# Performance work log

Hardware: AMD Instinct MI355X
Metric: run time of the kernel (lower is better)

## Reference

```python
import jax, jax.numpy as jnp
import numpy as np

B, N, K = 32, 64, 128          # batch, atoms per cell, channel width (128x0e + 128x1o)
R_MAX = 5.0
NUM_BESSEL = 8
P_CUT = 5                       # num_polynomial_cutoff
AVG_NEIGH = 16.0                # avg_num_neighbors
H_MLP = 512                     # hidden_dimensions_size, n_hidden_dimensions = 2
FEAT = 5 * K                    # ((num_interactions-1)*4 + 1) * 128 = 640


def silu(x):
    return x * jax.nn.sigmoid(x)


def _bessel_cutoff(r, mask):
    # Bessel radial basis * polynomial cutoff (MACE), masked on valid edges.
    n = jnp.arange(1, NUM_BESSEL + 1, dtype=r.dtype)
    rb = jnp.sqrt(2.0 / R_MAX) * jnp.sin(n * (jnp.pi / R_MAX) * r[..., None]) / r[..., None]
    u = r / R_MAX
    p = float(P_CUT)
    fc = 1.0 - 0.5 * (p + 1) * (p + 2) * u**P_CUT + p * (p + 2) * u**(P_CUT + 1) - 0.5 * p * (p + 1) * u**(P_CUT + 2)
    fc = fc * (u < 1.0)
    return rb * (fc * mask)[..., None]


def _sph(uvec):
    # Real spherical harmonics l=0,1,2 (component normalization), uvec: unit edge vectors.
    x, y, z = uvec[..., 0], uvec[..., 1], uvec[..., 2]
    s3, s5, s15 = 3.0**0.5, 5.0**0.5, 15.0**0.5
    Y0 = jnp.ones_like(x)[..., None]
    Y1 = jnp.stack([s3 * x, s3 * y, s3 * z], -1)
    Y2 = jnp.stack([s15 * x * y, s15 * y * z, 0.5 * s5 * (3 * z * z - 1.0),
                    s15 * x * z, 0.5 * s15 * (x * x - y * y)], -1)
    return Y0, Y1, Y2


def _radial_mlp(x, w0, b0, w1, b1, w2, b2, w3, b3):
    h = silu(x @ w0 + b0)
    h = silu(h @ w1 + b1)
    h = silu(h @ w2 + b2)
    return h @ w3 + b3


def setup_inputs() -> dict:
    key = jax.random.key(0)
    ks = jax.random.split(key, 32)
    f32 = jnp.float32

    def lin(k, fan_in, shape):
        return (jax.random.normal(k, shape, dtype=f32) / np.sqrt(fan_in)).astype(f32)

    inp = {
        "noisy_relative_positions": jax.random.uniform(ks[0], (B, N, 3), dtype=f32),
        "time": jax.random.uniform(ks[1], (B, 1), dtype=f32),
        "unit_cell": (11.0 * jnp.eye(3, dtype=f32) + 0.3 * jax.random.uniform(ks[2], (B, 3, 3), dtype=f32)),
        "w_embed": lin(ks[3], 1, (K,)),
        # interaction 1 radial MLP: 8 -> 64 -> 64 -> 64 -> 3*K (weights for l=0,1,2 paths)
        "r1_w0": lin(ks[4], NUM_BESSEL, (NUM_BESSEL, 64)), "r1_b0": jnp.zeros((64,), f32),
        "r1_w1": lin(ks[5], 64, (64, 64)), "r1_b1": jnp.zeros((64,), f32),
        "r1_w2": lin(ks[6], 64, (64, 64)), "r1_b2": jnp.zeros((64,), f32),
        "r1_w3": lin(ks[7], 64, (64, 3 * K)), "r1_b3": jnp.zeros((3 * K,), f32),
        "mix1_l0": lin(ks[8], K, (K, K)),
        "mix1_l1": lin(ks[9], K, (K, K)),
        "mix1_l2": lin(ks[10], K, (K, K)),
        # interaction 2 radial MLP: 8 -> 64 -> 64 -> 64 -> 2*K (paths 0e x 0e -> 0e, 1o x 1o -> 0e)
        "r2_w0": lin(ks[11], NUM_BESSEL, (NUM_BESSEL, 64)), "r2_b0": jnp.zeros((64,), f32),
        "r2_w1": lin(ks[12], 64, (64, 64)), "r2_b1": jnp.zeros((64,), f32),
        "r2_w2": lin(ks[13], 64, (64, 64)), "r2_b2": jnp.zeros((64,), f32),
        "r2_w3": lin(ks[14], 64, (64, 2 * K)), "r2_b3": jnp.zeros((2 * K,), f32),
        "mix2": lin(ks[15], K, (K, K)),
        # readout MLP: 641 -> 512 -> 512 -> 3
        "mlp_w0": lin(ks[16], FEAT + 1, (FEAT + 1, H_MLP)), "mlp_b0": jnp.zeros((H_MLP,), f32),
        "mlp_w1": lin(ks[17], H_MLP, (H_MLP, H_MLP)), "mlp_b1": jnp.zeros((H_MLP,), f32),
        "mlp_w2": lin(ks[18], H_MLP, (H_MLP, 3)), "mlp_b2": jnp.zeros((3,), f32),
    }
    return inp


def reference(noisy_relative_positions, time, unit_cell, w_embed,
              r1_w0, r1_b0, r1_w1, r1_b1, r1_w2, r1_b2, r1_w3, r1_b3,
              mix1_l0, mix1_l1, mix1_l2,
              r2_w0, r2_b0, r2_w1, r2_b1, r2_w2, r2_b2, r2_w3, r2_b3, mix2,
              mlp_w0, mlp_b0, mlp_w1, mlp_b1, mlp_w2, mlp_b2):
    frac = noisy_relative_positions                      # [B,N,3] fractional
    d = frac[:, :, None, :] - frac[:, None, :, :]        # [B,N,N,3]
    d = d - jnp.round(d)                                 # minimum-image PBC
    dc = jnp.einsum('bijc,bcd->bijd', d, unit_cell)      # cartesian displacements
    r = jnp.sqrt(jnp.maximum(jnp.sum(dc * dc, -1), 1e-12))
    mask = (r < R_MAX) & (~jnp.eye(N, dtype=bool))[None]
    r_safe = jnp.where(mask, r, 1.0)
    uvec = dc / r_safe[..., None] * mask[..., None]      # unit edge vectors (0 off-edge)

    rad = _bessel_cutoff(r_safe, mask)                   # [B,N,N,8]
    Y0, Y1, Y2 = _sph(uvec)                              # [B,N,N,1|3|5]

    h0 = jnp.broadcast_to(w_embed, (B, N, K))            # element embedding (single species)

    # ---- interaction 1: radial-weighted tensor product h_j (x) Y_l, scatter over j ----
    we = _radial_mlp(rad, r1_w0, r1_b0, r1_w1, r1_b1, r1_w2, r1_b2, r1_w3, r1_b3)
    we = we.reshape(B, N, N, 3, K) * mask[..., None, None]
    hj = h0[:, None, :, :]                               # sender features [B,1,N,K]
    msg0 = jnp.einsum('bijk,bijm->bimk', we[..., 0, :] * hj, Y0)[:, :, 0] / AVG_NEIGH  # [B,N,K]
    msg1 = jnp.einsum('bijk,bijm->bimk', we[..., 1, :] * hj, Y1) / AVG_NEIGH           # [B,N,3,K]
    msg2 = jnp.einsum('bijk,bijm->bimk', we[..., 2, :] * hj, Y2) / AVG_NEIGH           # [B,N,5,K]

    s1 = msg0 @ mix1_l0 + jnp.sum(msg2 * msg2, axis=2) @ mix1_l2   # scalars [B,N,K]
    v1 = jnp.einsum('bimk,kc->bimc', msg1, mix1_l1)                # vectors [B,N,3,K]
    h1 = silu(s1)

    # ---- interaction 2: scalar output from 0e x 0e and 1o x 1o -> 0e paths ----
    we2 = _radial_mlp(rad, r2_w0, r2_b0, r2_w1, r2_b1, r2_w2, r2_b2, r2_w3, r2_b3)
    we2 = we2.reshape(B, N, N, 2, K) * mask[..., None, None]
    msg_a = jnp.sum(we2[..., 0, :] * h1[:, None, :, :], axis=2)    # [B,N,K]
    inv = jnp.einsum('bijm,bjmk->bijk', Y1, v1)                    # Y1 . v1_j invariant
    msg_b = jnp.sum(we2[..., 1, :] * inv, axis=2)
    s2 = ((msg_a + msg_b) / AVG_NEIGH) @ mix2                      # [B,N,K]

    # node_feats: layer1 full irreps (128x0e + 128x1o -> 512) + layer2 scalars (128) = 640
    node_feats = jnp.concatenate([s1, v1.reshape(B, N, 3 * K), s2], axis=-1)

    t = jnp.broadcast_to(time[:, None, :], (B, N, 1))
    x = jnp.concatenate([node_feats, t], axis=-1)                  # [B,N,641]
    x = jax.nn.relu(x @ mlp_w0 + mlp_b0)
    x = jax.nn.relu(x @ mlp_w1 + mlp_b1)
    return x @ mlp_w2 + mlp_b2                                     # [B,N,3]
```

## Files before the change

kernel.cpp:

```cpp
#include <hip/hip_runtime.h>
#include <math.h>

#define B_ 32
#define N_ 64
#define K_ 128
#define NPAIR (B_*N_*N_)
#define PREP_TOTAL 733184

typedef __attribute__((ext_vector_type(8))) short short8;
typedef __attribute__((ext_vector_type(8))) __bf16 bf16x8;
typedef __attribute__((ext_vector_type(4))) float floatx4;

__device__ __forceinline__ float silu_f(float x) {
    return x / (1.0f + __expf(-x));
}

__device__ __forceinline__ short f2bf(float x) {
    union { float f; unsigned u; } v; v.f = x;
    unsigned r = (v.u + 0x7FFFu + ((v.u >> 16) & 1u)) >> 16;
    return (short)r;
}
__device__ __forceinline__ float bf2f(short s) {
    union { unsigned u; float f; } v;
    v.u = ((unsigned)(unsigned short)s) << 16;
    return v.f;
}
__device__ __forceinline__ bf16x8 ld_frag(const short* p) {
    short8 r = *(const short8*)p;
    return __builtin_bit_cast(bf16x8, r);
}

__global__ __launch_bounds__(256) void prep_kernel(
    const float* __restrict__ r1w1, const float* __restrict__ r1w2,
    const float* __restrict__ r2w1, const float* __restrict__ r2w2,
    const float* __restrict__ r2w3, const float* __restrict__ mw0,
    const float* __restrict__ mw1,
    const float* __restrict__ r1w0, const float* __restrict__ r2w0,
    const float* __restrict__ r1w3,
    const float* __restrict__ l0, const float* __restrict__ l1,
    const float* __restrict__ l2,
    short* __restrict__ dst)
{
    int idx = blockIdx.x * 256 + threadIdx.x;
    if (idx >= PREP_TOTAL) return;
    short v;
    if (idx < 4096) {
        int h = idx >> 6, k = idx & 63; v = f2bf(r1w1[k*64 + h]);
    } else if (idx < 8192) {
        int i = idx - 4096; int h = i >> 6, k = i & 63; v = f2bf(r1w2[k*64 + h]);
    } else if (idx < 12288) {
        int i = idx - 8192; int h = i >> 6, k = i & 63; v = f2bf(r2w1[k*64 + h]);
    } else if (idx < 16384) {
        int i = idx - 12288; int h = i >> 6, k = i & 63; v = f2bf(r2w2[k*64 + h]);
    } else if (idx < 32768) {
        int i = idx - 16384; int col = i >> 6, h = i & 63; v = f2bf(r2w3[h*256 + col]);
    } else if (idx < 393216) {
        int i = idx - 32768; int n = i / 704, k = i - n*704;
        v = (k < 641) ? f2bf(mw0[(size_t)k*512 + n]) : (short)0;
    } else if (idx < 655360) {
        int i = idx - 393216; int n = i >> 9, k = i & 511;
        v = f2bf(mw1[(size_t)k*512 + n]);
    } else if (idx < 657408) {
        int i = idx - 655360; int h = i >> 5, k = i & 31;
        v = (k < 8) ? f2bf(r1w0[k*64 + h]) : (short)0;
    } else if (idx < 659456) {
        int i = idx - 657408; int h = i >> 5, k = i & 31;
        v = (k < 8) ? f2bf(r2w0[k*64 + h]) : (short)0;
    } else if (idx < 684032) {
        int i = idx - 659456; int col = i >> 6, h = i & 63;
        v = f2bf(r1w3[(size_t)h*384 + col]);
    } else {
        int i = idx - 684032; int n = i >> 7, k = i & 127;
        float src = (n < 128) ? l0[(size_t)k*128 + n]
                  : (n < 256) ? l1[(size_t)k*128 + (n-128)]
                              : l2[(size_t)k*128 + (n-256)];
        v = f2bf(src);
    }
    dst[idx] = v;
}

__device__ __forceinline__ void mfma_layer(
    const short* __restrict__ src, const short* __restrict__ WT,
    const float* __restrict__ bias, short* __restrict__ dst,
    int wv, int qd, int nn)
{
    floatx4 acc[4];
    #pragma unroll
    for (int tt = 0; tt < 4; tt++) acc[tt] = (floatx4){0.f, 0.f, 0.f, 0.f};
    #pragma unroll
    for (int ks = 0; ks < 64; ks += 32) {
        bf16x8 a = ld_frag(&src[(wv*16 + nn)*72 + ks + qd*8]);
        #pragma unroll
        for (int tt = 0; tt < 4; tt++) {
            bf16x8 b = ld_frag(&WT[(tt*16 + nn)*64 + ks + qd*8]);
            acc[tt] = __builtin_amdgcn_mfma_f32_16x16x32_bf16(a, b, acc[tt], 0, 0, 0);
        }
    }
    #pragma unroll
    for (int tt = 0; tt < 4; tt++) {
        int col = tt*16 + nn;
        float bv = bias[col];
        #pragma unroll
        for (int i = 0; i < 4; i++) {
            int row = wv*16 + qd*4 + i;
            dst[row*72 + col] = f2bf(silu_f(acc[tt][i] + bv));
        }
    }
}

__device__ __forceinline__ void mfma_layer_T(
    const short* __restrict__ src, const short* __restrict__ WT,
    const float* __restrict__ bias, short* __restrict__ dstT,
    int wv, int qd, int nn)
{
    floatx4 acc[4];
    #pragma unroll
    for (int tt = 0; tt < 4; tt++) acc[tt] = (floatx4){0.f, 0.f, 0.f, 0.f};
    #pragma unroll
    for (int ks = 0; ks < 64; ks += 32) {
        bf16x8 a = ld_frag(&src[(wv*16 + nn)*72 + ks + qd*8]);
        #pragma unroll
        for (int tt = 0; tt < 4; tt++) {
            bf16x8 b = ld_frag(&WT[(tt*16 + nn)*64 + ks + qd*8]);
            acc[tt] = __builtin_amdgcn_mfma_f32_16x16x32_bf16(a, b, acc[tt], 0, 0, 0);
        }
    }
    #pragma unroll
    for (int tt = 0; tt < 4; tt++) {
        int col = tt*16 + nn;
        float bv = bias[col];
        #pragma unroll
        for (int i = 0; i < 4; i++) {
            int row = wv*16 + qd*4 + i;
            dstT[col*72 + row] = f2bf(silu_f(acc[tt][i] + bv));
        }
    }
}

__device__ __forceinline__ void mfma_layer_gout(
    const short* __restrict__ src, const short* __restrict__ WT,
    const float* __restrict__ bias, short* __restrict__ gdst,
    int wv, int qd, int nn)
{
    floatx4 acc[4];
    #pragma unroll
    for (int tt = 0; tt < 4; tt++) acc[tt] = (floatx4){0.f, 0.f, 0.f, 0.f};
    #pragma unroll
    for (int ks = 0; ks < 64; ks += 32) {
        bf16x8 a = ld_frag(&src[(wv*16 + nn)*72 + ks + qd*8]);
        #pragma unroll
        for (int tt = 0; tt < 4; tt++) {
            bf16x8 b = ld_frag(&WT[(tt*16 + nn)*64 + ks + qd*8]);
            acc[tt] = __builtin_amdgcn_mfma_f32_16x16x32_bf16(a, b, acc[tt], 0, 0, 0);
        }
    }
    #pragma unroll
    for (int tt = 0; tt < 4; tt++) {
        int col = tt*16 + nn;
        float bv = bias[col];
        #pragma unroll
        for (int i = 0; i < 4; i++) {
            int row = wv*16 + qd*4 + i;
            gdst[row*64 + col] = f2bf(silu_f(acc[tt][i] + bv));
        }
    }
}

__device__ __forceinline__ void mfma_layer0(
    const short* __restrict__ rad_bf, const short* __restrict__ w0T,
    const float* __restrict__ b0, short* __restrict__ dst,
    int wv, int qd, int nn)
{
    floatx4 acc[4];
    #pragma unroll
    for (int tt = 0; tt < 4; tt++) acc[tt] = (floatx4){0.f, 0.f, 0.f, 0.f};
    bf16x8 a = ld_frag(&rad_bf[(wv*16 + nn)*32 + qd*8]);
    #pragma unroll
    for (int tt = 0; tt < 4; tt++) {
        bf16x8 b = ld_frag(&w0T[(tt*16 + nn)*32 + qd*8]);
        acc[tt] = __builtin_amdgcn_mfma_f32_16x16x32_bf16(a, b, acc[tt], 0, 0, 0);
    }
    #pragma unroll
    for (int tt = 0; tt < 4; tt++) {
        int col = tt*16 + nn;
        float bv = b0[col];
        #pragma unroll
        for (int i = 0; i < 4; i++) {
            int row = wv*16 + qd*4 + i;
            dst[row*72 + col] = f2bf(silu_f(acc[tt][i] + bv));
        }
    }
}

__global__ __launch_bounds__(256) void mlpx_kernel(
    const float* __restrict__ pos, const float* __restrict__ cell,
    const short* __restrict__ w0T1, const float* __restrict__ b01,
    const short* __restrict__ w1T1, const float* __restrict__ b11,
    const short* __restrict__ w2T1, const float* __restrict__ b21,
    const short* __restrict__ w0T2, const float* __restrict__ b02,
    const short* __restrict__ w1T2, const float* __restrict__ b12,
    const short* __restrict__ w2T2, const float* __restrict__ b22,
    float* __restrict__ geo4, short* __restrict__ hc2, short* __restrict__ Gg)
{
    __shared__ __align__(16) short actA[64*72];
    __shared__ __align__(16) short actB[64*72];
    __shared__ __align__(16) short rad_bf[64*32];
    __shared__ __align__(16) short Ym_bf[16*72];
    int t = threadIdx.x;
    int wv = t >> 6, lane = t & 63, qd = lane >> 4, nn = lane & 15;
    int node = blockIdx.x;
    int b = node >> 6;
    int irow = node & 63;
    size_t pbase = (size_t)node * 64;

    if (t < 64) {
        int j = t;
        const float* pi = pos + (size_t)(b*N_ + irow)*3;
        const float* pj = pos + (size_t)(b*N_ + j)*3;
        float d0 = pi[0]-pj[0], d1 = pi[1]-pj[1], d2 = pi[2]-pj[2];
        d0 -= rintf(d0); d1 -= rintf(d1); d2 -= rintf(d2);
        const float* C = cell + b*9;
        float dc0 = d0*C[0] + d1*C[3] + d2*C[6];
        float dc1 = d0*C[1] + d1*C[4] + d2*C[7];
        float dc2 = d0*C[2] + d1*C[5] + d2*C[8];
        float r2 = fmaxf(dc0*dc0 + dc1*dc1 + dc2*dc2, 1e-12f);
        float r = sqrtf(r2);
        bool m = (r < 5.0f) && (irow != j);
        float mf = m ? 1.0f : 0.0f;
        float rs = m ? r : 1.0f;
        float inv_rs = 1.0f / rs;
        float x = dc0*inv_rs*mf, y = dc1*inv_rs*mf, z = dc2*inv_rs*mf;
        float u = r * 0.2f;
        float u2 = u*u, u4 = u2*u2, u5 = u4*u;
        float fc = 1.0f - 21.0f*u5 + 35.0f*u5*u - 15.0f*u5*u2;
        fc = (u < 1.0f) ? fc : 0.0f;
        float pref = 0.6324555320336759f * inv_rs * (fc * mf);
        float w = 0.6283185307179586f * rs;
        float sw = sinf(w), cw = cosf(w);
        float twoc = 2.0f * cw;
        float sm = 0.0f, s = sw;
        #pragma unroll
        for (int n = 0; n < 8; n++) {
            rad_bf[j*32 + n] = f2bf(pref * s);
            float nx = twoc*s - sm;
            sm = s; s = nx;
        }
        #pragma unroll
        for (int k = 8; k < 32; k++) rad_bf[j*32 + k] = 0;
        const float s3  = 1.7320508075688772f;
        const float s5  = 2.23606797749979f;
        const float s15 = 3.872983346207417f;
        float vals[9];
        vals[0] = mf;
        vals[1] = s3*x; vals[2] = s3*y; vals[3] = s3*z;
        vals[4] = s15*x*y;
        vals[5] = s15*y*z;
        vals[6] = 0.5f*s5*(3.0f*z*z - 1.0f);
        vals[7] = s15*x*z;
        vals[8] = 0.5f*s15*(x*x - y*y);
        *(float4*)&geo4[(pbase + j)*4] = make_float4(mf, vals[1], vals[2], vals[3]);
        #pragma unroll
        for (int m9 = 0; m9 < 9; m9++) Ym_bf[m9*72 + j] = f2bf(vals[m9]);
        #pragma unroll
        for (int m9 = 9; m9 < 16; m9++) Ym_bf[m9*72 + j] = 0;
        #pragma unroll
        for (int m9 = 0; m9 < 9; m9++) {
            float sv = vals[m9];
            #pragma unroll
            for (int off = 32; off > 0; off >>= 1) sv += __shfl_xor(sv, off);
            if (j == m9)
                *(float*)(Gg + (size_t)node*1152 + m9*72 + 64) = sv;
        }
    }
    __syncthreads();

    mfma_layer0(rad_bf, w0T2, b02, actA, wv, qd, nn);
    __syncthreads();

    mfma_layer(actA, w1T2, b12, actB, wv, qd, nn);
    __syncthreads();

    mfma_layer_gout(actB, w2T2, b22, hc2 + (size_t)node*4096, wv, qd, nn);
    mfma_layer0(rad_bf, w0T1, b01, actA, wv, qd, nn);
    __syncthreads();

    mfma_layer(actA, w1T1, b11, actB, wv, qd, nn);
    __syncthreads();

    mfma_layer_T(actB, w2T1, b21, actA, wv, qd, nn);
    __syncthreads();

    {
        floatx4 acc = (floatx4){0.f, 0.f, 0.f, 0.f};
        #pragma unroll
        for (int ks = 0; ks < 64; ks += 32) {
            bf16x8 a = ld_frag(&Ym_bf[nn*72 + ks + qd*8]);
            bf16x8 bb = ld_frag(&actA[(wv*16 + nn)*72 + ks + qd*8]);
            acc = __builtin_amdgcn_mfma_f32_16x16x32_bf16(a, bb, acc, 0, 0, 0);
        }
        #pragma unroll
        for (int i = 0; i < 4; i++)
            Gg[(size_t)node*1152 + (qd*4 + i)*72 + wv*16 + nn] = f2bf(acc[i]);
    }
}

__global__ __launch_bounds__(256) void back1_kernel(
    const float* __restrict__ wemb,
    const short* __restrict__ Gg,
    const short* __restrict__ w3T, const float* __restrict__ b3,
    const short* __restrict__ lcatT, const float* __restrict__ timeg,
    float* __restrict__ h1g, float* __restrict__ v1g, short* __restrict__ featsb)
{
    __shared__ __align__(16) short G_lds[16*72];
    __shared__ __align__(16) short A2[16*136];
    __shared__ float q_s[128];
    __shared__ float Ps[256];
    int t = threadIdx.x;
    int wv = t >> 6, lane = t & 63, qd = lane >> 4, nn = lane & 15;
    int node = blockIdx.x;
    int b = node >> 6;

    if (t < 144)
        ((uint4*)G_lds)[t] = ((const uint4*)(Gg + (size_t)node*1152))[t];
    if (t < 128) q_s[t] = 0.f;
    for (int z = 680 + t; z < 2176; z += 256) A2[z] = 0;
    __syncthreads();

    {
        bf16x8 ga0 = ld_frag(&G_lds[nn*72 + qd*8]);
        bf16x8 ga1 = ld_frag(&G_lds[nn*72 + 32 + qd*8]);
        floatx4 acc[6];
        #pragma unroll
        for (int tt = 0; tt < 6; tt++) acc[tt] = (floatx4){0.f, 0.f, 0.f, 0.f};
        #pragma unroll
        for (int tt = 0; tt < 6; tt++) {
            int tn = wv*6 + tt;
            bf16x8 b0f = ld_frag(&w3T[(tn*16 + nn)*64 + qd*8]);
            bf16x8 b1f = ld_frag(&w3T[(tn*16 + nn)*64 + 32 + qd*8]);
            acc[tt] = __builtin_amdgcn_mfma_f32_16x16x32_bf16(ga0, b0f, acc[tt], 0, 0, 0);
            acc[tt] = __builtin_amdgcn_mfma_f32_16x16x32_bf16(ga1, b1f, acc[tt], 0, 0, 0);
        }
        #pragma unroll
        for (int tt = 0; tt < 6; tt++) {
            int col = (wv*6 + tt)*16 + nn;
            #pragma unroll
            for (int i = 0; i < 4; i++) {
                int m9 = qd*4 + i;
                if (m9 < 9) {
                    int c = (m9 == 0) ? 0 : ((m9 < 4) ? 1 : 2);
                    int k = col - c*128;
                    if (k >= 0 && k < 128) {
                        float sym = *(const float*)(&G_lds[m9*72 + 64]);
                        float val = (acc[tt][i] + sym*b3[col]) * wemb[k] * 0.0625f;
                        if (m9 == 0)      A2[k] = f2bf(val);
                        else if (m9 < 4)  A2[(m9+1)*136 + k] = f2bf(val);
                        else              atomicAdd(&q_s[k], val*val);
                    }
                }
            }
        }
    }
    __syncthreads();

    if (t < 128) A2[136 + t] = f2bf(q_s[t]);
    __syncthreads();

    {
        bf16x8 pa[4];
        #pragma unroll
        for (int ksI = 0; ksI < 4; ksI++)
            pa[ksI] = ld_frag(&A2[nn*136 + ksI*32 + qd*8]);
        floatx4 acc[6];
        #pragma unroll
        for (int tt = 0; tt < 6; tt++) acc[tt] = (floatx4){0.f, 0.f, 0.f, 0.f};
        #pragma unroll
        for (int tt = 0; tt < 6; tt++) {
            int tn = wv*6 + tt;
            #pragma unroll
            for (int ksI = 0; ksI < 4; ksI++) {
                bf16x8 bf = ld_frag(&lcatT[((size_t)(tn*16 + nn))*128 + ksI*32 + qd*8]);
                acc[tt] = __builtin_amdgcn_mfma_f32_16x16x32_bf16(pa[ksI], bf, acc[tt], 0, 0, 0);
            }
        }
        #pragma unroll
        for (int tt = 0; tt < 6; tt++) {
            int n = (wv*6 + tt)*16 + nn;
            #pragma unroll
            for (int i = 0; i < 4; i++) {
                int r = qd*4 + i;
                float val = acc[tt][i];
                if (r == 0 && n < 128) Ps[n] = val;
                else if (r == 1 && n >= 256) Ps[128 + n - 256] = val;
                else if (r >= 2 && r < 5 && n >= 128 && n < 256) {
                    int m9 = r - 2, cc = n - 128;
                    v1g[(size_t)node*384 + m9*128 + cc] = val;
                    featsb[(size_t)node*704 + 128 + m9*128 + cc] = f2bf(val);
                }
            }
        }
    }
    __syncthreads();

    if (t < 128) {
        float s1 = Ps[t] + Ps[128 + t];
        featsb[(size_t)node*704 + t] = f2bf(s1);
        h1g[(size_t)node*128 + t] = silu_f(s1);
    } else if (t == 128) {
        featsb[(size_t)node*704 + 640] = f2bf(timeg[b]);
    } else if (t > 128 && t < 192) {
        featsb[(size_t)node*704 + 640 + (t - 128)] = 0;
    }
}

__global__ __launch_bounds__(256) void pass2b_kernel(
    const float* __restrict__ geo4,
    const short* __restrict__ hc2,
    const short* __restrict__ w3T, const float* __restrict__ b3,
    const float* __restrict__ mix2,
    const float* __restrict__ h1g, const float* __restrict__ v1g,
    short* __restrict__ featsb)
{
    __shared__ float mask_s[64];
    __shared__ float Y1s[64*4];
    __shared__ float msgab[128];
    int t = threadIdx.x;
    int wv = t >> 6, lane = t & 63, qd = lane >> 4, nn = lane & 15;
    int node = blockIdx.x;
    int b = node >> 6;
    size_t pbase = (size_t)node * 64;

    if (t < 64) {
        float4 g = *(const float4*)&geo4[(pbase + t)*4];
        mask_s[t] = g.x;
        Y1s[t*4 + 0] = g.y; Y1s[t*4 + 1] = g.z; Y1s[t*4 + 2] = g.w;
    }
    if (t >= 64 && t < 192) msgab[t - 64] = 0.f;
    __syncthreads();

    const short* hcb = hc2 + (size_t)node*4096;
    bf16x8 a0 = ld_frag(&hcb[(wv*16 + nn)*64 + qd*8]);
    bf16x8 a1 = ld_frag(&hcb[(wv*16 + nn)*64 + 32 + qd*8]);
    for (int g = 0; g < 4; g++) {
        floatx4 acc[4];
        #pragma unroll
        for (int tt = 0; tt < 4; tt++) acc[tt] = (floatx4){0.f, 0.f, 0.f, 0.f};
        #pragma unroll
        for (int tt = 0; tt < 4; tt++) {
            int ct = g*4 + tt;
            bf16x8 b0f = ld_frag(&w3T[(ct*16 + nn)*64 + qd*8]);
            bf16x8 b1f = ld_frag(&w3T[(ct*16 + nn)*64 + 32 + qd*8]);
            acc[tt] = __builtin_amdgcn_mfma_f32_16x16x32_bf16(a0, b0f, acc[tt], 0, 0, 0);
            acc[tt] = __builtin_amdgcn_mfma_f32_16x16x32_bf16(a1, b1f, acc[tt], 0, 0, 0);
        }
        #pragma unroll
        for (int tt = 0; tt < 4; tt++) {
            int col = (g*4 + tt)*16 + nn;
            float bias = b3[col];
            int k = col & 127;
            float p = 0.f;
            if (col < 128) {
                #pragma unroll
                for (int i = 0; i < 4; i++) {
                    int j = wv*16 + qd*4 + i;
                    float we = (acc[tt][i] + bias) * mask_s[j];
                    p += we * h1g[((size_t)b*64 + j)*128 + k];
                }
            } else {
                #pragma unroll
                for (int i = 0; i < 4; i++) {
                    int j = wv*16 + qd*4 + i;
                    float we = (acc[tt][i] + bias) * mask_s[j];
                    const float* vb = &v1g[((size_t)b*64 + j)*384 + k];
                    float inv = Y1s[j*4+0]*vb[0] + Y1s[j*4+1]*vb[128] + Y1s[j*4+2]*vb[256];
                    p += we * inv;
                }
            }
            p += __shfl_xor(p, 16);
            p += __shfl_xor(p, 32);
            if (qd == 0) atomicAdd(&msgab[k], p);
        }
    }
    __syncthreads();

    if (t < 128) {
        int c = t;
        float acc = 0.f;
        for (int k = 0; k < 128; k++) acc += msgab[k] * mix2[k*128 + c];
        featsb[(size_t)node*704 + 512 + c] = f2bf(acc * 0.0625f);
    }
}

__global__ __launch_bounds__(256) void gemm_mfma_kernel(
    const short* __restrict__ A, int lda,
    const short* __restrict__ BT, int ldb, int K,
    const float* __restrict__ bias, short* __restrict__ Cout, int ldo)
{
    __shared__ short As[64*72];
    __shared__ short Bs[64*72];
    int t = threadIdx.x;
    int wv = t >> 6, lane = t & 63, qd = lane >> 4, nn = lane & 15;
    int m0 = blockIdx.x * 64, n0 = blockIdx.y * 64;
    floatx4 acc[4];
    #pragma unroll
    for (int tt = 0; tt < 4; tt++) acc[tt] = (floatx4){0.f, 0.f, 0.f, 0.f};

    for (int kc = 0; kc < K; kc += 64) {
        for (int s = t; s < 512; s += 256) {
            int j = s >> 3, kk = (s & 7) * 8;
            *(uint4*)&As[j*72 + kk] = *(const uint4*)&A[(size_t)(m0 + j)*lda + kc + kk];
            *(uint4*)&Bs[j*72 + kk] = *(const uint4*)&BT[(size_t)(n0 + j)*ldb + kc + kk];
        }
        __syncthreads();
        #pragma unroll
        for (int ks = 0; ks < 64; ks += 32) {
            bf16x8 a = ld_frag(&As[(wv*16 + nn)*72 + ks + qd*8]);
            #pragma unroll
            for (int tt = 0; tt < 4; tt++) {
                bf16x8 bb = ld_frag(&Bs[(tt*16 + nn)*72 + ks + qd*8]);
                acc[tt] = __builtin_amdgcn_mfma_f32_16x16x32_bf16(a, bb, acc[tt], 0, 0, 0);
            }
        }
        __syncthreads();
    }
    #pragma unroll
    for (int tt = 0; tt < 4; tt++) {
        int n = n0 + tt*16 + nn;
        float bv = bias[n];
        #pragma unroll
        for (int i = 0; i < 4; i++) {
            int m = m0 + wv*16 + qd*4 + i;
            Cout[(size_t)m*ldo + n] = f2bf(fmaxf(acc[tt][i] + bv, 0.f));
        }
    }
}

__global__ __launch_bounds__(64) void final3_kernel(
    const short* __restrict__ H, const float* __restrict__ w2,
    const float* __restrict__ b2, float* __restrict__ out)
{
    int node = blockIdx.x, lane = threadIdx.x;
    float a0 = 0.f, a1 = 0.f, a2 = 0.f;
    #pragma unroll
    for (int r = 0; r < 8; r++) {
        int k = r*64 + lane;
        float h = bf2f(H[(size_t)node*512 + k]);
        a0 += h * w2[k*3 + 0];
        a1 += h * w2[k*3 + 1];
        a2 += h * w2[k*3 + 2];
    }
    #pragma unroll
    for (int off = 32; off > 0; off >>= 1) {
        a0 += __shfl_down(a0, off);
        a1 += __shfl_down(a1, off);
        a2 += __shfl_down(a2, off);
    }
    if (lane == 0) {
        out[(size_t)node*3 + 0] = a0 + b2[0];
        out[(size_t)node*3 + 1] = a1 + b2[1];
        out[(size_t)node*3 + 2] = a2 + b2[2];
    }
}

extern "C" void kernel_launch(void* const* d_in, const int* in_sizes, int n_in,
                              void* d_out, int out_size, void* d_ws, size_t ws_size,
                              hipStream_t stream) {
    const float* pos   = (const float*)d_in[0];
    const float* timeg = (const float*)d_in[1];
    const float* cell  = (const float*)d_in[2];
    const float* wemb  = (const float*)d_in[3];
    const float* r1w0  = (const float*)d_in[4];
    const float* r1b0  = (const float*)d_in[5];
    const float* r1w1  = (const float*)d_in[6];
    const float* r1b1  = (const float*)d_in[7];
    const float* r1w2  = (const float*)d_in[8];
    const float* r1b2  = (const float*)d_in[9];
    const float* r1w3  = (const float*)d_in[10];
    const float* r1b3  = (const float*)d_in[11];
    const float* l0    = (const float*)d_in[12];
    const float* l1    = (const float*)d_in[13];
    const float* l2    = (const float*)d_in[14];
    const float* r2w0  = (const float*)d_in[15];
    const float* r2b0  = (const float*)d_in[16];
    const float* r2w1  = (const float*)d_in[17];
    const float* r2b1  = (const float*)d_in[18];
    const float* r2w2  = (const float*)d_in[19];
    const float* r2b2  = (const float*)d_in[20];
    const float* r2w3  = (const float*)d_in[21];
    const float* r2b3  = (const float*)d_in[22];
    const float* mix2  = (const float*)d_in[23];
    const float* mw0   = (const float*)d_in[24];
    const float* mb0   = (const float*)d_in[25];
    const float* mw1   = (const float*)d_in[26];
    const float* mb1   = (const float*)d_in[27];
    const float* mw2   = (const float*)d_in[28];
    const float* mb2   = (const float*)d_in[29];

    float* ws    = (float*)d_ws;
    float* geo4  = ws;
    float* h1    = geo4 + (size_t)NPAIR*4;
    float* v1    = h1   + (size_t)B_*N_*K_;
    short* featsb = (short*)(v1 + (size_t)B_*N_*3*K_);
    short* prep  = featsb + (size_t)2048*704;
    short* w1T_1 = prep;
    short* w2T_1 = prep + 4096;
    short* w1T_2 = prep + 8192;
    short* w2T_2 = prep + 12288;
    short* w3T_2 = prep + 16384;
    short* wT0   = prep + 32768;
    short* wT1   = prep + 393216;
    short* w0T_1 = prep + 655360;
    short* w0T_2 = prep + 657408;
    short* w3T_1 = prep + 659456;
    short* lcatT = prep + 684032;
    short* hc2   = prep + PREP_TOTAL;
    short* Gg    = hc2 + (size_t)2048*4096;
    short* h0bb  = hc2;
    short* h1bb  = hc2 + (size_t)2048*512;

    prep_kernel<<<(PREP_TOTAL + 255)/256, 256, 0, stream>>>(
        r1w1, r1w2, r2w1, r2w2, r2w3, mw0, mw1,
        r1w0, r2w0, r1w3, l0, l1, l2, prep);
    mlpx_kernel<<<B_*N_, 256, 0, stream>>>(pos, cell,
        w0T_1, r1b0, w1T_1, r1b1, w2T_1, r1b2,
        w0T_2, r2b0, w1T_2, r2b1, w2T_2, r2b2,
        geo4, hc2, Gg);
    back1_kernel<<<B_*N_, 256, 0, stream>>>(wemb, Gg,
        w3T_1, r1b3, lcatT, timeg, h1, v1, featsb);
    pass2b_kernel<<<B_*N_, 256, 0, stream>>>(geo4, hc2,
        w3T_2, r2b3, mix2, h1, v1, featsb);
    dim3 g0(32, 8);
    gemm_mfma_kernel<<<g0, 256, 0, stream>>>(featsb, 704, wT0, 704, 704, mb0, h0bb, 512);
    gemm_mfma_kernel<<<g0, 256, 0, stream>>>(h0bb, 512, wT1, 512, 512, mb1, h1bb, 512);
    final3_kernel<<<B_*N_, 64, 0, stream>>>(h1bb, mw2, mb2, (float*)d_out);
}
```

Measured before the change: 289.1 us.

## Merge all stages into one persistent cooperative kernel with grid syncs

The seven separate launches (weight prep, radial MLPs, two interaction passes, two GEMMs, final projection) become one persistent cooperative kernel. Blocks loop over nodes or tiles in each stage and are separated by grid-wide barriers, with shared memory carved from one buffer. The aim is to remove per-launch overhead and the tail gaps between kernels. In exchange, the grid is capped at occupancy times 256 CUs, so each block handles several nodes serially and every stage is bound by the slowest block before the barrier. If the cooperative launch fails, the original multi-kernel path runs instead.

```diff
diff --git a/kernel.cpp b/kernel.cpp
--- a/kernel.cpp
+++ b/kernel.cpp
@@ -1,5 +1,8 @@
 #include <hip/hip_runtime.h>
+#include <hip/hip_cooperative_groups.h>
 #include <math.h>
+
+namespace cg = cooperative_groups;
 
 #define B_ 32
 #define N_ 64
@@ -30,7 +33,8 @@
     return __builtin_bit_cast(bf16x8, r);
 }
 
-__global__ __launch_bounds__(256) void prep_kernel(
+
+__device__ __forceinline__ void prep_elem(int idx,
     const float* __restrict__ r1w1, const float* __restrict__ r1w2,
     const float* __restrict__ r2w1, const float* __restrict__ r2w2,
     const float* __restrict__ r2w3, const float* __restrict__ mw0,
@@ -41,8 +45,6 @@
     const float* __restrict__ l2,
     short* __restrict__ dst)
 {
-    int idx = blockIdx.x * 256 + threadIdx.x;
-    if (idx >= PREP_TOTAL) return;
     short v;
     if (idx < 4096) {
         int h = idx >> 6, k = idx & 63; v = f2bf(r1w1[k*64 + h]);
@@ -192,7 +194,7 @@
     }
 }
 
-__global__ __launch_bounds__(256) void mlpx_kernel(
+__device__ __forceinline__ void mlpx_body(int node, char* sm,
     const float* __restrict__ pos, const float* __restrict__ cell,
     const short* __restrict__ w0T1, const float* __restrict__ b01,
     const short* __restrict__ w1T1, const float* __restrict__ b11,
@@ -202,16 +204,18 @@
     const short* __restrict__ w2T2, const float* __restrict__ b22,
     float* __restrict__ geo4, short* __restrict__ hc2, short* __restrict__ Gg)
 {
-    __shared__ __align__(16) short actA[64*72];
-    __shared__ __align__(16) short actB[64*72];
-    __shared__ __align__(16) short rad_bf[64*32];
-    __shared__ __align__(16) short Ym_bf[16*72];
+    short* actA   = (short*)sm;
+    short* actB   = (short*)(sm + 9216);
+    short* rad_bf = (short*)(sm + 18432);
+    short* Ym_bf  = (short*)(sm + 22528);
+
     int t = threadIdx.x;
     int wv = t >> 6, lane = t & 63, qd = lane >> 4, nn = lane & 15;
-    int node = blockIdx.x;
     int b = node >> 6;
     int irow = node & 63;
     size_t pbase = (size_t)node * 64;
+
+    __syncthreads();
 
     if (t < 64) {
         int j = t;
@@ -238,12 +242,12 @@
         float w = 0.6283185307179586f * rs;
         float sw = sinf(w), cw = cosf(w);
         float twoc = 2.0f * cw;
-        float sm = 0.0f, s = sw;
+        float sm2 = 0.0f, s = sw;
         #pragma unroll
         for (int n = 0; n < 8; n++) {
             rad_bf[j*32 + n] = f2bf(pref * s);
-            float nx = twoc*s - sm;
-            sm = s; s = nx;
+            float nx = twoc*s - sm2;
+            sm2 = s; s = nx;
         }
         #pragma unroll
         for (int k = 8; k < 32; k++) rad_bf[j*32 + k] = 0;
@@ -276,20 +280,15 @@
 
     mfma_layer0(rad_bf, w0T2, b02, actA, wv, qd, nn);
     __syncthreads();
-
     mfma_layer(actA, w1T2, b12, actB, wv, qd, nn);
     __syncthreads();
-
     mfma_layer_gout(actB, w2T2, b22, hc2 + (size_t)node*4096, wv, qd, nn);
     mfma_layer0(rad_bf, w0T1, b01, actA, wv, qd, nn);
     __syncthreads();
-
     mfma_layer(actA, w1T1, b11, actB, wv, qd, nn);
     __syncthreads();
-
     mfma_layer_T(actB, w2T1, b21, actA, wv, qd, nn);
     __syncthreads();
-
     {
         floatx4 acc = (floatx4){0.f, 0.f, 0.f, 0.f};
         #pragma unroll
@@ -304,21 +303,22 @@
     }
 }
 
-__global__ __launch_bounds__(256) void back1_kernel(
+__device__ __forceinline__ void back1_body(int node, char* sm,
     const float* __restrict__ wemb,
     const short* __restrict__ Gg,
     const short* __restrict__ w3T, const float* __restrict__ b3,
     const short* __restrict__ lcatT, const float* __restrict__ timeg,
     float* __restrict__ h1g, float* __restrict__ v1g, short* __restrict__ featsb)
 {
-    __shared__ __align__(16) short G_lds[16*72];
-    __shared__ __align__(16) short A2[16*136];
-    __shared__ float q_s[128];
-    __shared__ float Ps[256];
+    short* G_lds = (short*)sm;
+    short* A2    = (short*)(sm + 2304);
+    float* q_s   = (float*)(sm + 6656);
+    float* Ps    = (float*)(sm + 7168);
     int t = threadIdx.x;
     int wv = t >> 6, lane = t & 63, qd = lane >> 4, nn = lane & 15;
-    int node = blockIdx.x;
     int b = node >> 6;
+
+    __syncthreads();
 
     if (t < 144)
         ((uint4*)G_lds)[t] = ((const uint4*)(Gg + (size_t)node*1152))[t];
@@ -412,7 +412,7 @@
     }
 }
 
-__global__ __launch_bounds__(256) void pass2b_kernel(
+__device__ __forceinline__ void pass2b_body(int node, char* sm,
     const float* __restrict__ geo4,
     const short* __restrict__ hc2,
     const short* __restrict__ w3T, const float* __restrict__ b3,
@@ -420,14 +420,15 @@
     const float* __restrict__ h1g, const float* __restrict__ v1g,
     short* __restrict__ featsb)
 {
-    __shared__ float mask_s[64];
-    __shared__ float Y1s[64*4];
-    __shared__ float msgab[128];
+    float* mask_s = (float*)sm;
+    float* Y1s    = (float*)(sm + 256);
+    float* msgab  = (float*)(sm + 1280);
     int t = threadIdx.x;
     int wv = t >> 6, lane = t & 63, qd = lane >> 4, nn = lane & 15;
-    int node = blockIdx.x;
     int b = node >> 6;
     size_t pbase = (size_t)node * 64;
+
+    __syncthreads();
 
     if (t < 64) {
         float4 g = *(const float4*)&geo4[(pbase + t)*4];
@@ -490,21 +491,21 @@
     }
 }
 
-__global__ __launch_bounds__(256) void gemm_mfma_kernel(
+__device__ __forceinline__ void gemm_body(int m0, int n0, char* sm,
     const short* __restrict__ A, int lda,
     const short* __restrict__ BT, int ldb, int K,
     const float* __restrict__ bias, short* __restrict__ Cout, int ldo)
 {
-    __shared__ short As[64*72];
-    __shared__ short Bs[64*72];
+    short* As = (short*)sm;
+    short* Bs = (short*)(sm + 9216);
     int t = threadIdx.x;
     int wv = t >> 6, lane = t & 63, qd = lane >> 4, nn = lane & 15;
-    int m0 = blockIdx.x * 64, n0 = blockIdx.y * 64;
     floatx4 acc[4];
     #pragma unroll
     for (int tt = 0; tt < 4; tt++) acc[tt] = (floatx4){0.f, 0.f, 0.f, 0.f};
 
     for (int kc = 0; kc < K; kc += 64) {
+        __syncthreads();
         for (int s = t; s < 512; s += 256) {
             int j = s >> 3, kk = (s & 7) * 8;
             *(uint4*)&As[j*72 + kk] = *(const uint4*)&A[(size_t)(m0 + j)*lda + kc + kk];
@@ -520,8 +521,8 @@
                 acc[tt] = __builtin_amdgcn_mfma_f32_16x16x32_bf16(a, bb, acc[tt], 0, 0, 0);
             }
         }
-        __syncthreads();
-    }
+    }
+    __syncthreads();
     #pragma unroll
     for (int tt = 0; tt < 4; tt++) {
         int n = n0 + tt*16 + nn;
@@ -534,11 +535,10 @@
     }
 }
 
-__global__ __launch_bounds__(64) void final3_kernel(
+__device__ __forceinline__ void final3_body(int node, int lane,
     const short* __restrict__ H, const float* __restrict__ w2,
     const float* __restrict__ b2, float* __restrict__ out)
 {
-    int node = blockIdx.x, lane = threadIdx.x;
     float a0 = 0.f, a1 = 0.f, a2 = 0.f;
     #pragma unroll
     for (int r = 0; r < 8; r++) {
@@ -558,6 +558,146 @@
         out[(size_t)node*3 + 0] = a0 + b2[0];
         out[(size_t)node*3 + 1] = a1 + b2[1];
         out[(size_t)node*3 + 2] = a2 + b2[2];
+    }
+}
+
+__global__ __launch_bounds__(256) void prep_kernel(
+    const float* r1w1, const float* r1w2, const float* r2w1, const float* r2w2,
+    const float* r2w3, const float* mw0, const float* mw1,
+    const float* r1w0, const float* r2w0, const float* r1w3,
+    const float* l0, const float* l1, const float* l2, short* dst)
+{
+    int idx = blockIdx.x * 256 + threadIdx.x;
+    if (idx >= PREP_TOTAL) return;
+    prep_elem(idx, r1w1, r1w2, r2w1, r2w2, r2w3, mw0, mw1, r1w0, r2w0, r1w3,
+              l0, l1, l2, dst);
+}
+
+__global__ __launch_bounds__(256) void mlpx_kernel(
+    const float* pos, const float* cell,
+    const short* w0T1, const float* b01, const short* w1T1, const float* b11,
+    const short* w2T1, const float* b21,
+    const short* w0T2, const float* b02, const short* w1T2, const float* b12,
+    const short* w2T2, const float* b22,
+    float* geo4, short* hc2, short* Gg)
+{
+    __shared__ __align__(16) char sm[24832];
+    mlpx_body(blockIdx.x, sm, pos, cell, w0T1, b01, w1T1, b11, w2T1, b21,
+              w0T2, b02, w1T2, b12, w2T2, b22, geo4, hc2, Gg);
+}
+
+__global__ __launch_bounds__(256) void back1_kernel(
+    const float* wemb, const short* Gg, const short* w3T, const float* b3,
+    const short* lcatT, const float* timeg,
+    float* h1g, float* v1g, short* featsb)
+{
+    __shared__ __align__(16) char sm[8192];
+    back1_body(blockIdx.x, sm, wemb, Gg, w3T, b3, lcatT, timeg, h1g, v1g, featsb);
+}
+
+__global__ __launch_bounds__(256) void pass2b_kernel(
+    const float* geo4, const short* hc2, const short* w3T, const float* b3,
+    const float* mix2, const float* h1g, const float* v1g, short* featsb)
+{
+    __shared__ __align__(16) char sm[1792];
+    pass2b_body(blockIdx.x, sm, geo4, hc2, w3T, b3, mix2, h1g, v1g, featsb);
+}
+
+__global__ __launch_bounds__(256) void gemm_mfma_kernel(
+    const short* A, int lda, const short* BT, int ldb, int K,
+    const float* bias, short* Cout, int ldo)
+{
+    __shared__ __align__(16) char sm[18432];
+    gemm_body(blockIdx.x * 64, blockIdx.y * 64, sm, A, lda, BT, ldb, K, bias, Cout, ldo);
+}
+
+__global__ __launch_bounds__(64) void final3_kernel(
+    const short* H, const float* w2, const float* b2, float* out)
+{
+    final3_body(blockIdx.x, threadIdx.x, H, w2, b2, out);
+}
+
+__global__ __launch_bounds__(256) void mega_kernel(
+    const float* pos, const float* timeg, const float* cell, const float* wemb,
+    const float* r1w0, const float* r1b0, const float* r1w1, const float* r1b1,
+    const float* r1w2, const float* r1b2, const float* r1w3, const float* r1b3,
+    const float* l0, const float* l1, const float* l2,
+    const float* r2w0, const float* r2b0, const float* r2w1, const float* r2b1,
+    const float* r2w2, const float* r2b2, const float* r2w3, const float* r2b3,
+    const float* mix2,
+    const float* mw0, const float* mb0, const float* mw1, const float* mb1,
+    const float* mw2, const float* mb2,
+    float* ws, float* outp)
+{
+    cg::grid_group grid = cg::this_grid();
+    __shared__ __align__(16) char sm[24832];
+    const int G = (int)gridDim.x;
+    int t = threadIdx.x;
+
+    float* geo4  = ws;
+    float* h1    = geo4 + (size_t)NPAIR*4;
+    float* v1    = h1   + (size_t)B_*N_*K_;
+    short* featsb = (short*)(v1 + (size_t)B_*N_*3*K_);
+    short* prep  = featsb + (size_t)2048*704;
+    short* w1T_1 = prep;
+    short* w2T_1 = prep + 4096;
+    short* w1T_2 = prep + 8192;
+    short* w2T_2 = prep + 12288;
+    short* w3T_2 = prep + 16384;
+    short* wT0   = prep + 32768;
+    short* wT1   = prep + 393216;
+    short* w0T_1 = prep + 655360;
+    short* w0T_2 = prep + 657408;
+    short* w3T_1 = prep + 659456;
+    short* lcatT = prep + 684032;
+    short* hc2   = prep + PREP_TOTAL;
+    short* Gg    = hc2 + (size_t)2048*4096;
+    short* h0bb  = hc2;
+    short* h1bb  = hc2 + (size_t)2048*512;
+
+    for (int idx = blockIdx.x*256 + t; idx < PREP_TOTAL; idx += G*256)
+        prep_elem(idx, r1w1, r1w2, r2w1, r2w2, r2w3, mw0, mw1, r1w0, r2w0, r1w3,
+                  l0, l1, l2, prep);
+    __threadfence();
+    grid.sync();
+
+    for (int node = blockIdx.x; node < 2048; node += G)
+        mlpx_body(node, sm, pos, cell, w0T_1, r1b0, w1T_1, r1b1, w2T_1, r1b2,
+                  w0T_2, r2b0, w1T_2, r2b1, w2T_2, r2b2, geo4, hc2, Gg);
+    __threadfence();
+    grid.sync();
+
+    for (int node = blockIdx.x; node < 2048; node += G)
+        back1_body(node, sm, wemb, Gg, w3T_1, r1b3, lcatT, timeg, h1, v1, featsb);
+    __threadfence();
+    grid.sync();
+
+    for (int node = blockIdx.x; node < 2048; node += G)
+        pass2b_body(node, sm, geo4, hc2, w3T_2, r2b3, mix2, h1, v1, featsb);
+    __threadfence();
+    grid.sync();
+
+    for (int tile = blockIdx.x; tile < 256; tile += G) {
+        int m0 = (tile & 31) * 64, n0 = (tile >> 5) * 64;
+        gemm_body(m0, n0, sm, featsb, 704, wT0, 704, 704, mb0, h0bb, 512);
+    }
+    __threadfence();
+    grid.sync();
+
+    for (int tile = blockIdx.x; tile < 256; tile += G) {
+        int m0 = (tile & 31) * 64, n0 = (tile >> 5) * 64;
+        gemm_body(m0, n0, sm, h0bb, 512, wT1, 512, 512, mb1, h1bb, 512);
+    }
+    __threadfence();
+    grid.sync();
+
+    {
+        int wv = t >> 6, lane = t & 63;
+        for (int base = blockIdx.x*4; base < 2048; base += G*4) {
+            int node = base + wv;
+            if (node < 2048)
+                final3_body(node, lane, h1bb, mw2, mb2, outp);
+        }
     }
 }
 
@@ -596,6 +736,7 @@
     const float* mb2   = (const float*)d_in[29];
 
     float* ws    = (float*)d_ws;
+    float* outp  = (float*)d_out;
     float* geo4  = ws;
     float* h1    = geo4 + (size_t)NPAIR*4;
     float* v1    = h1   + (size_t)B_*N_*K_;
@@ -617,19 +758,48 @@
     short* h0bb  = hc2;
     short* h1bb  = hc2 + (size_t)2048*512;
 
-    prep_kernel<<<(PREP_TOTAL + 255)/256, 256, 0, stream>>>(
-        r1w1, r1w2, r2w1, r2w2, r2w3, mw0, mw1,
-        r1w0, r2w0, r1w3, l0, l1, l2, prep);
-    mlpx_kernel<<<B_*N_, 256, 0, stream>>>(pos, cell,
-        w0T_1, r1b0, w1T_1, r1b1, w2T_1, r1b2,
-        w0T_2, r2b0, w1T_2, r2b1, w2T_2, r2b2,
-        geo4, hc2, Gg);
-    back1_kernel<<<B_*N_, 256, 0, stream>>>(wemb, Gg,
-        w3T_1, r1b3, lcatT, timeg, h1, v1, featsb);
-    pass2b_kernel<<<B_*N_, 256, 0, stream>>>(geo4, hc2,
-        w3T_2, r2b3, mix2, h1, v1, featsb);
-    dim3 g0(32, 8);
-    gemm_mfma_kernel<<<g0, 256, 0, stream>>>(featsb, 704, wT0, 704, 704, mb0, h0bb, 512);
-    gemm_mfma_kernel<<<g0, 256, 0, stream>>>(h0bb, 512, wT1, 512, 512, mb1, h1bb, 512);
-    final3_kernel<<<B_*N_, 64, 0, stream>>>(h1bb, mw2, mb2, (float*)d_out);
-}
+    static int coopGrid = -1;
+    if (coopGrid < 0) {
+        int nb = 0;
+        hipError_t qe = hipOccupancyMaxActiveBlocksPerMultiprocessor(
+            &nb, (const void*)mega_kernel, 256, 0);
+        if (qe != hipSuccess || nb < 1) nb = 1;
+        long g = (long)nb * 256;
+        if (g > 2048) g = 2048;
+        coopGrid = (int)g;
+    }
+
+    void* margs[] = {
+        (void*)&pos, (void*)&timeg, (void*)&cell, (void*)&wemb,
+        (void*)&r1w0, (void*)&r1b0, (void*)&r1w1, (void*)&r1b1,
+        (void*)&r1w2, (void*)&r1b2, (void*)&r1w3, (void*)&r1b3,
+        (void*)&l0, (void*)&l1, (void*)&l2,
+        (void*)&r2w0, (void*)&r2b0, (void*)&r2w1, (void*)&r2b1,
+        (void*)&r2w2, (void*)&r2b2, (void*)&r2w3, (void*)&r2b3,
+        (void*)&mix2,
+        (void*)&mw0, (void*)&mb0, (void*)&mw1, (void*)&mb1,
+        (void*)&mw2, (void*)&mb2,
+        (void*)&ws, (void*)&outp
+    };
+
+    hipError_t err = hipLaunchCooperativeKernel(
+        (const void*)mega_kernel, dim3(coopGrid), dim3(256), margs, 0, stream);
+
+    if (err != hipSuccess) {
+        prep_kernel<<<(PREP_TOTAL + 255)/256, 256, 0, stream>>>(
+            r1w1, r1w2, r2w1, r2w2, r2w3, mw0, mw1,
+            r1w0, r2w0, r1w3, l0, l1, l2, prep);
+        mlpx_kernel<<<B_*N_, 256, 0, stream>>>(pos, cell,
+            w0T_1, r1b0, w1T_1, r1b1, w2T_1, r1b2,
+            w0T_2, r2b0, w1T_2, r2b1, w2T_2, r2b2,
+            geo4, hc2, Gg);
+        back1_kernel<<<B_*N_, 256, 0, stream>>>(wemb, Gg,
+            w3T_1, r1b3, lcatT, timeg, h1, v1, featsb);
+        pass2b_kernel<<<B_*N_, 256, 0, stream>>>(geo4, hc2,
+            w3T_2, r2b3, mix2, h1, v1, featsb);
+        dim3 g0(32, 8);
+        gemm_mfma_kernel<<<g0, 256, 0, stream>>>(featsb, 704, wT0, 704, 704, mb0, h0bb, 512);
+        gemm_mfma_kernel<<<g0, 256, 0, stream>>>(h0bb, 512, wT1, 512, 512, mb1, h1bb, 512);
+        final3_kernel<<<B_*N_, 64, 0, stream>>>(h1bb, mw2, mb2, outp);
+    }
+}
```

Result: slower. 763.3 us (+164.0%).

## Transpose h1/v1 layouts for vector loads and use single-wave GEMM tiles

Applied to the files above, without the earlier changes.

h1 is now stored transposed per batch (channel-major, atom-minor) and v1 is interleaved with its three vector components padded to four. This lets pass2b read four neighbour values or three components with one float4 load instead of scattered scalar loads. The MLP GEMMs move from 256-thread LDS-tiled blocks to 64-thread waves that load fragments directly from global memory over 16-row tiles, which raises block count and removes LDS staging and barriers. The cost is less operand reuse across waves and more redundant global traffic for the B matrix.

```diff
diff --git a/kernel.cpp b/kernel.cpp
--- a/kernel.cpp
+++ b/kernel.cpp
@@ -238,12 +238,12 @@
         float w = 0.6283185307179586f * rs;
         float sw = sinf(w), cw = cosf(w);
         float twoc = 2.0f * cw;
-        float sm = 0.0f, s = sw;
+        float sm2 = 0.0f, s = sw;
         #pragma unroll
         for (int n = 0; n < 8; n++) {
             rad_bf[j*32 + n] = f2bf(pref * s);
-            float nx = twoc*s - sm;
-            sm = s; s = nx;
+            float nx = twoc*s - sm2;
+            sm2 = s; s = nx;
         }
         #pragma unroll
         for (int k = 8; k < 32; k++) rad_bf[j*32 + k] = 0;
@@ -276,20 +276,15 @@
 
     mfma_layer0(rad_bf, w0T2, b02, actA, wv, qd, nn);
     __syncthreads();
-
     mfma_layer(actA, w1T2, b12, actB, wv, qd, nn);
     __syncthreads();
-
     mfma_layer_gout(actB, w2T2, b22, hc2 + (size_t)node*4096, wv, qd, nn);
     mfma_layer0(rad_bf, w0T1, b01, actA, wv, qd, nn);
     __syncthreads();
-
     mfma_layer(actA, w1T1, b11, actB, wv, qd, nn);
     __syncthreads();
-
     mfma_layer_T(actB, w2T1, b21, actA, wv, qd, nn);
     __syncthreads();
-
     {
         floatx4 acc = (floatx4){0.f, 0.f, 0.f, 0.f};
         #pragma unroll
@@ -309,7 +304,7 @@
     const short* __restrict__ Gg,
     const short* __restrict__ w3T, const float* __restrict__ b3,
     const short* __restrict__ lcatT, const float* __restrict__ timeg,
-    float* __restrict__ h1g, float* __restrict__ v1g, short* __restrict__ featsb)
+    float* __restrict__ h1t, float* __restrict__ v1g, short* __restrict__ featsb)
 {
     __shared__ __align__(16) short G_lds[16*72];
     __shared__ __align__(16) short A2[16*136];
@@ -319,6 +314,7 @@
     int wv = t >> 6, lane = t & 63, qd = lane >> 4, nn = lane & 15;
     int node = blockIdx.x;
     int b = node >> 6;
+    int irow = node & 63;
 
     if (t < 144)
         ((uint4*)G_lds)[t] = ((const uint4*)(Gg + (size_t)node*1152))[t];
@@ -393,7 +389,7 @@
                 else if (r == 1 && n >= 256) Ps[128 + n - 256] = val;
                 else if (r >= 2 && r < 5 && n >= 128 && n < 256) {
                     int m9 = r - 2, cc = n - 128;
-                    v1g[(size_t)node*384 + m9*128 + cc] = val;
+                    v1g[((size_t)node*128 + cc)*4 + m9] = val;
                     featsb[(size_t)node*704 + 128 + m9*128 + cc] = f2bf(val);
                 }
             }
@@ -404,7 +400,7 @@
     if (t < 128) {
         float s1 = Ps[t] + Ps[128 + t];
         featsb[(size_t)node*704 + t] = f2bf(s1);
-        h1g[(size_t)node*128 + t] = silu_f(s1);
+        h1t[((size_t)b*128 + t)*64 + irow] = silu_f(s1);
     } else if (t == 128) {
         featsb[(size_t)node*704 + 640] = f2bf(timeg[b]);
     } else if (t > 128 && t < 192) {
@@ -417,7 +413,7 @@
     const short* __restrict__ hc2,
     const short* __restrict__ w3T, const float* __restrict__ b3,
     const float* __restrict__ mix2,
-    const float* __restrict__ h1g, const float* __restrict__ v1g,
+    const float* __restrict__ h1t, const float* __restrict__ v1g,
     short* __restrict__ featsb)
 {
     __shared__ float mask_s[64];
@@ -440,6 +436,7 @@
     const short* hcb = hc2 + (size_t)node*4096;
     bf16x8 a0 = ld_frag(&hcb[(wv*16 + nn)*64 + qd*8]);
     bf16x8 a1 = ld_frag(&hcb[(wv*16 + nn)*64 + 32 + qd*8]);
+    int j0 = wv*16 + qd*4;
     for (int g = 0; g < 4; g++) {
         floatx4 acc[4];
         #pragma unroll
@@ -459,19 +456,20 @@
             int k = col & 127;
             float p = 0.f;
             if (col < 128) {
+                float4 hv = *(const float4*)&h1t[((size_t)b*128 + k)*64 + j0];
                 #pragma unroll
                 for (int i = 0; i < 4; i++) {
-                    int j = wv*16 + qd*4 + i;
+                    int j = j0 + i;
                     float we = (acc[tt][i] + bias) * mask_s[j];
-                    p += we * h1g[((size_t)b*64 + j)*128 + k];
+                    p += we * ((const float*)&hv)[i];
                 }
             } else {
                 #pragma unroll
                 for (int i = 0; i < 4; i++) {
-                    int j = wv*16 + qd*4 + i;
+                    int j = j0 + i;
                     float we = (acc[tt][i] + bias) * mask_s[j];
-                    const float* vb = &v1g[((size_t)b*64 + j)*384 + k];
-                    float inv = Y1s[j*4+0]*vb[0] + Y1s[j*4+1]*vb[128] + Y1s[j*4+2]*vb[256];
+                    float4 vb = *(const float4*)&v1g[(((size_t)b*64 + j)*128 + k)*4];
+                    float inv = Y1s[j*4+0]*vb.x + Y1s[j*4+1]*vb.y + Y1s[j*4+2]*vb.z;
                     p += we * inv;
                 }
             }
@@ -490,37 +488,28 @@
     }
 }
 
-__global__ __launch_bounds__(256) void gemm_mfma_kernel(
+__global__ __launch_bounds__(64) void gemm_wave_kernel(
     const short* __restrict__ A, int lda,
     const short* __restrict__ BT, int ldb, int K,
     const float* __restrict__ bias, short* __restrict__ Cout, int ldo)
 {
-    __shared__ short As[64*72];
-    __shared__ short Bs[64*72];
-    int t = threadIdx.x;
-    int wv = t >> 6, lane = t & 63, qd = lane >> 4, nn = lane & 15;
-    int m0 = blockIdx.x * 64, n0 = blockIdx.y * 64;
+    int lane = threadIdx.x;
+    int qd = lane >> 4, nn = lane & 15;
+    int m0 = blockIdx.x * 16, n0 = blockIdx.y * 64;
     floatx4 acc[4];
     #pragma unroll
     for (int tt = 0; tt < 4; tt++) acc[tt] = (floatx4){0.f, 0.f, 0.f, 0.f};
 
-    for (int kc = 0; kc < K; kc += 64) {
-        for (int s = t; s < 512; s += 256) {
-            int j = s >> 3, kk = (s & 7) * 8;
-            *(uint4*)&As[j*72 + kk] = *(const uint4*)&A[(size_t)(m0 + j)*lda + kc + kk];
-            *(uint4*)&Bs[j*72 + kk] = *(const uint4*)&BT[(size_t)(n0 + j)*ldb + kc + kk];
-        }
-        __syncthreads();
-        #pragma unroll
-        for (int ks = 0; ks < 64; ks += 32) {
-            bf16x8 a = ld_frag(&As[(wv*16 + nn)*72 + ks + qd*8]);
-            #pragma unroll
-            for (int tt = 0; tt < 4; tt++) {
-                bf16x8 bb = ld_frag(&Bs[(tt*16 + nn)*72 + ks + qd*8]);
-                acc[tt] = __builtin_amdgcn_mfma_f32_16x16x32_bf16(a, bb, acc[tt], 0, 0, 0);
-            }
-        }
-        __syncthreads();
+    const short* arow  = A  + (size_t)(m0 + nn)*lda + qd*8;
+    const short* bbase = BT + (size_t)(n0 + nn)*ldb + qd*8;
+    #pragma unroll 2
+    for (int kc = 0; kc < K; kc += 32) {
+        bf16x8 a = ld_frag(arow + kc);
+        #pragma unroll
+        for (int tt = 0; tt < 4; tt++) {
+            bf16x8 bb = ld_frag(bbase + (size_t)tt*16*ldb + kc);
+            acc[tt] = __builtin_amdgcn_mfma_f32_16x16x32_bf16(a, bb, acc[tt], 0, 0, 0);
+        }
     }
     #pragma unroll
     for (int tt = 0; tt < 4; tt++) {
@@ -528,7 +517,7 @@
         float bv = bias[n];
         #pragma unroll
         for (int i = 0; i < 4; i++) {
-            int m = m0 + wv*16 + qd*4 + i;
+            int m = m0 + qd*4 + i;
             Cout[(size_t)m*ldo + n] = f2bf(fmaxf(acc[tt][i] + bv, 0.f));
         }
     }
@@ -597,9 +586,9 @@
 
     float* ws    = (float*)d_ws;
     float* geo4  = ws;
-    float* h1    = geo4 + (size_t)NPAIR*4;
-    float* v1    = h1   + (size_t)B_*N_*K_;
-    short* featsb = (short*)(v1 + (size_t)B_*N_*3*K_);
+    float* h1t   = geo4 + (size_t)NPAIR*4;
+    float* v1    = h1t + (size_t)B_*K_*N_;
+    short* featsb = (short*)(v1 + (size_t)2048*128*4);
     short* prep  = featsb + (size_t)2048*704;
     short* w1T_1 = prep;
     short* w2T_1 = prep + 4096;
@@ -625,11 +614,11 @@
         w0T_2, r2b0, w1T_2, r2b1, w2T_2, r2b2,
         geo4, hc2, Gg);
     back1_kernel<<<B_*N_, 256, 0, stream>>>(wemb, Gg,
-        w3T_1, r1b3, lcatT, timeg, h1, v1, featsb);
+        w3T_1, r1b3, lcatT, timeg, h1t, v1, featsb);
     pass2b_kernel<<<B_*N_, 256, 0, stream>>>(geo4, hc2,
-        w3T_2, r2b3, mix2, h1, v1, featsb);
-    dim3 g0(32, 8);
-    gemm_mfma_kernel<<<g0, 256, 0, stream>>>(featsb, 704, wT0, 704, 704, mb0, h0bb, 512);
-    gemm_mfma_kernel<<<g0, 256, 0, stream>>>(h0bb, 512, wT1, 512, 512, mb1, h1bb, 512);
+        w3T_2, r2b3, mix2, h1t, v1, featsb);
+    dim3 g1(128, 8);
+    gemm_wave_kernel<<<g1, 64, 0, stream>>>(featsb, 704, wT0, 704, 704, mb0, h0bb, 512);
+    gemm_wave_kernel<<<g1, 64, 0, stream>>>(h0bb, 512, wT1, 512, 512, mb1, h1bb, 512);
     final3_kernel<<<B_*N_, 64, 0, stream>>>(h1bb, mw2, mb2, (float*)d_out);
 }
```

Result: slower. 308.0 us (+6.6%).
